# Kernel tuning notes

Hardware: AMD Instinct MI355X
Metric: run time of the kernel (lower is better)

The kernel has to match this reference:

```python
import jax, jax.numpy as jnp
import numpy as np
from math import factorial

LMAX = 4
N_COEFF = (LMAX + 1) ** 2      # 25 real spherical-harmonic coefficients
N_RADII = 300                  # distance_bins
N_NODES = 512
FEAT = 128
RES_BETA, RES_ALPHA = 180, 360
DIST_STEP = 0.05


def _sh_basis(lmax, y, alpha):
    """Real spherical harmonics evaluated on a (beta, alpha) product grid.
    y = cos(beta) quadrature nodes. Returns [res_beta, res_alpha, (lmax+1)^2]."""
    B, A = len(y), len(alpha)
    P = np.zeros((lmax + 1, lmax + 1, B))
    P[0, 0] = 1.0
    s = np.sqrt(np.clip(1.0 - y * y, 0.0, None))
    for m in range(1, lmax + 1):
        P[m, m] = -(2 * m - 1) * s * P[m - 1, m - 1]
    for m in range(lmax):
        P[m + 1, m] = (2 * m + 1) * y * P[m, m]
    for m in range(lmax + 1):
        for l in range(m + 2, lmax + 1):
            P[l, m] = ((2 * l - 1) * y * P[l - 1, m] - (l + m - 1) * P[l - 2, m]) / (l - m)
    cols = []
    for l in range(lmax + 1):
        for m in range(-l, l + 1):
            am = abs(m)
            Nlm = np.sqrt((2 * l + 1) / (4 * np.pi) * factorial(l - am) / factorial(l + am))
            if m == 0:
                col = Nlm * P[l, 0][:, None] * np.ones((1, A))
            elif m > 0:
                col = np.sqrt(2.0) * Nlm * P[l, m][:, None] * np.cos(m * alpha)[None, :]
            else:
                col = np.sqrt(2.0) * Nlm * P[l, am][:, None] * np.sin(am * alpha)[None, :]
            cols.append(col)
    return np.stack(cols, axis=-1).astype(np.float32)


def setup_inputs() -> dict:
    key = jax.random.key(0)
    ks = jax.random.split(key, 14)

    def lin(k, a, b):
        return jax.random.normal(k, (a, b), jnp.float32) / np.float32(np.sqrt(a))

    x = jax.random.normal(ks[0], (N_NODES, FEAT), jnp.float32)
    fd = [FEAT, 128, 128, 64, 16, 2]
    td = [FEAT, 128, 128, 128, 128, 128, 6]
    fW = [lin(ks[1 + i], fd[i], fd[i + 1]) for i in range(5)]
    tW = [lin(ks[6 + i], td[i], td[i + 1]) for i in range(6)]
    pos_w = lin(ks[12], 2 * FEAT, N_RADII * N_COEFF)
    type_emb = jax.random.normal(ks[13], (5, FEAT), jnp.float32)

    y_np, w_np = np.polynomial.legendre.leggauss(RES_BETA)
    alpha_np = np.linspace(0.0, 2.0 * np.pi, RES_ALPHA, endpoint=False)
    basis = jnp.asarray(_sh_basis(LMAX, y_np, alpha_np))          # [B, A, C]
    qw = jnp.asarray(w_np / 2.0, jnp.float32)                     # gausslegendre / 2
    y_grid = jnp.asarray(y_np, jnp.float32)
    alpha_grid = jnp.asarray(alpha_np, jnp.float32)

    return {
        "x": x,
        "focus_w1": fW[0], "focus_w2": fW[1], "focus_w3": fW[2], "focus_w4": fW[3], "focus_w5": fW[4],
        "type_w1": tW[0], "type_w2": tW[1], "type_w3": tW[2], "type_w4": tW[3], "type_w5": tW[4], "type_w6": tW[5],
        "pos_w": pos_w, "type_emb": type_emb,
        "basis": basis, "qw": qw, "y_grid": y_grid, "alpha_grid": alpha_grid,
        "res_beta": RES_BETA, "res_alpha": RES_ALPHA,
    }


def reference(x, focus_w1, focus_w2, focus_w3, focus_w4, focus_w5,
              type_w1, type_w2, type_w3, type_w4, type_w5, type_w6,
              pos_w, type_emb, basis, qw, y_grid, alpha_grid,
              res_beta, res_alpha):
    n_nodes = x.shape[0]

    # --- focus MLP (relu), per-node logits; STOP logit 0 appended ---
    h = x
    for W in (focus_w1, focus_w2, focus_w3, focus_w4):
        h = jax.nn.relu(h @ W)
    focus_scores = (h @ focus_w5)[:, 0]                             # [n_nodes]
    focus_probs = jax.nn.softmax(jnp.concatenate([focus_scores, jnp.zeros((1,), x.dtype)]))
    focus = jnp.minimum(jnp.argmax(focus_probs), n_nodes - 1)

    # --- type MLP (softplus) on the focus node's features ---
    feat_f = x[focus]                                               # [128]
    th = feat_f
    for W in (type_w1, type_w2, type_w3, type_w4, type_w5):
        th = jax.nn.softplus(th @ W)
    type_dist = jax.nn.softmax(th @ type_w6)                        # [6]
    type_idx = jnp.minimum(jnp.argmax(type_dist), 4)

    # --- position head: SH coefficients per radial shell ---
    pos_in = jnp.concatenate([feat_f, type_emb[type_idx]])          # [256]
    coeffs = (pos_in @ pos_w).reshape(N_RADII, N_COEFF)             # [R, C]

    # to_s2grid: log-density on the sphere for every radial shell
    f = jnp.einsum('rc,bac->rba', coeffs, basis)                    # [R, B, A]
    log_meas = jnp.log(qw)[:, None] + jnp.log(2.0 * jnp.pi / res_alpha)  # [B, 1]

    # radial distribution: integral of exp(f) over the sphere, per shell
    log_radial = jax.nn.logsumexp(f + log_meas[None], axis=(1, 2))  # [R]
    radial_probs = jax.nn.softmax(log_radial)

    key = jax.random.key(42)
    k_r, k_a = jax.random.split(key)
    r_idx = jax.random.categorical(k_r, log_radial)

    # angular distribution at the sampled radius, normalized on S2
    fr = f[r_idx]                                                   # [B, A]
    logZr = jax.nn.logsumexp(fr + log_meas)
    angular_dist = jnp.exp(fr - logZr)                              # [B, A]

    joint_log = (fr + log_meas - logZr).reshape(-1)
    idx = jax.random.categorical(k_a, joint_log)
    y_i = idx // res_alpha
    a_i = idx % res_alpha

    radius_pred = (r_idx.astype(jnp.float32) + 1.0) * DIST_STEP
    return (type_dist, radial_probs, angular_dist, radius_pred, y_grid[y_i], alpha_grid[a_i])
```

## Files before the change

kernel.cpp:

```cpp
#include <hip/hip_runtime.h>
#include <math.h>
#include <stdint.h>

#define NNODES 512
#define FEAT   128
#define NR     300
#define NC     25
#define NB     180
#define NA     360
#define RSPLIT 4
#define BCHUNK (NB / RSPLIT)
#define O_TYPE   0
#define O_RAD    6
#define O_ANG    306
#define O_RADIUS 65106
#define O_Y      65107
#define O_ALPHA  65108

#define WS_KEYS   0
#define WS_FOCUS  4
#define WS_TYPEI  5
#define WS_RIDX   6
#define WS_INVZ   7
#define WS_DEAD   8
#define WS_SCORES 320
#define WS_POSIN  832
#define WS_PSUM   1088
#define WS_PV     1280
#define WS_PI     1472
#define WS_Q      1664
#define WS_HR     6176
#define WS_COEF   8352
#define WS_LRP    15872

#define GB_MLP   NNODES
#define GB_PREP  36
#define GB_PFT   162
#define GB_PFP   768
#define GB_TOTAL (GB_MLP + GB_PREP + GB_PFT + GB_PFP)

__constant__ int c_m_of_c[25] = {0,-1,0,1,-2,-1,0,1,2,-3,-2,-1,0,1,2,3,-4,-3,-2,-1,0,1,2,3,4};
__constant__ int c_h_cnt[9] = {5,4,3,2,1,4,3,2,1};
__constant__ int c_h_idx[9][5] = {
  {0,2,6,12,20},
  {3,7,13,21,0},
  {8,14,22,0,0},
  {15,23,0,0,0},
  {24,0,0,0,0},
  {1,5,11,19,0},
  {4,10,18,0,0},
  {9,17,0,0,0},
  {16,0,0,0,0}};

__device__ __forceinline__ void tf2x32(uint32_t k0, uint32_t k1, uint32_t x0, uint32_t x1,
                                       uint32_t& o0, uint32_t& o1) {
  uint32_t ks2 = k0 ^ k1 ^ 0x1BD11BDAu;
#define TF_RND(r) { x0 += x1; x1 = (x1 << r) | (x1 >> (32 - r)); x1 ^= x0; }
  x0 += k0; x1 += k1;
  TF_RND(13) TF_RND(15) TF_RND(26) TF_RND(6)
  x0 += k1; x1 += ks2 + 1u;
  TF_RND(17) TF_RND(29) TF_RND(16) TF_RND(24)
  x0 += ks2; x1 += k0 + 2u;
  TF_RND(13) TF_RND(15) TF_RND(26) TF_RND(6)
  x0 += k0; x1 += k1 + 3u;
  TF_RND(17) TF_RND(29) TF_RND(16) TF_RND(24)
  x0 += k1; x1 += ks2 + 4u;
  TF_RND(13) TF_RND(15) TF_RND(26) TF_RND(6)
  x0 += ks2; x1 += k0 + 5u;
#undef TF_RND
  o0 = x0; o1 = x1;
}

__device__ __forceinline__ float gumbel32(uint32_t k0, uint32_t k1, uint32_t lo) {
  uint32_t o0, o1; tf2x32(k0, k1, 0u, lo, o0, o1);
  uint32_t bits = o0 ^ o1;
  float u = __uint_as_float((bits >> 9) | 0x3f800000u) - 1.0f;
  u = fmaxf(u, 1.1754944e-38f);
  return -logf(-logf(u));
}

__global__ __launch_bounds__(128) void k_front(const float* __restrict__ x,
    const float* __restrict__ w1, const float* __restrict__ w2, const float* __restrict__ w3,
    const float* __restrict__ w4, const float* __restrict__ w5,
    const float* __restrict__ basis, const float* __restrict__ alpha_grid,
    const float* __restrict__ tw1, const float* __restrict__ tw2, const float* __restrict__ tw3,
    const float* __restrict__ tw4, const float* __restrict__ tw5, const float* __restrict__ tw6,
    const float* __restrict__ pos_w,
    float* __restrict__ wsf) {
  int bx = blockIdx.x;
  if (bx >= GB_MLP + GB_PREP + GB_PFT) {
    int pb = bx - (GB_MLP + GB_PREP + GB_PFT);
    const float4* p4 = (const float4*)pos_w;
    const int n4 = NR * NC * 256 / 4;
    float acc = 0.f;
    for (int i = pb * 128 + threadIdx.x; i < n4; i += GB_PFP * 128) {
      float4 v = p4[i];
      acc += v.x + v.y + v.z + v.w;
    }
    if (acc == -1.2345678e30f) wsf[WS_DEAD] = acc;
    return;
  }
  if (bx >= GB_MLP + GB_PREP) {
    int pb = bx - (GB_MLP + GB_PREP);
    int base = pb * 128;
    float acc = 0.f;
    int i = base + threadIdx.x;
    const float4* mats[5] = {(const float4*)tw1, (const float4*)tw2, (const float4*)tw3,
                             (const float4*)tw4, (const float4*)tw5};
    int mi = pb >> 5;
    if (mi < 5) {
      int li = (pb & 31) * 128 + threadIdx.x;
      float4 v = mats[mi][li];
      acc += v.x + v.y + v.z + v.w;
    } else {
      int li = (pb - 160) * 128 + threadIdx.x;
      if (li < 192) { float4 v = ((const float4*)tw6)[li]; acc += v.x + v.y + v.z + v.w; }
    }
    (void)i;
    if (acc == -1.2345678e30f) wsf[WS_DEAD] = acc;
    return;
  }
  if (bx >= GB_MLP) {
    int t = (bx - GB_MLP) * 128 + threadIdx.x;
    if (bx == GB_MLP && threadIdx.x == 0) {
      uint32_t* wu = (uint32_t*)wsf;
      uint32_t o0, o1;
      tf2x32(0u, 42u, 0u, 0u, o0, o1); wu[WS_KEYS + 0] = o0; wu[WS_KEYS + 1] = o1;
      tf2x32(0u, 42u, 0u, 1u, o0, o1); wu[WS_KEYS + 2] = o0; wu[WS_KEYS + 3] = o1;
    }
    if (t < NB * NC) {
      int b = t / NC, c = t % NC;
      int m = c_m_of_c[c];
      float q;
      if (m >= 0) {
        q = basis[(b * NA + 0) * NC + c];
      } else {
        float a10 = alpha_grid[10];
        q = basis[(b * NA + 10) * NC + c] / sinf((float)(-m) * a10);
      }
      wsf[WS_Q + t] = q;
    }
    return;
  }
  __shared__ float ha[128], hb[128];
  int n = bx, j = threadIdx.x;
  ha[j] = x[n * FEAT + j];
  __syncthreads();
  float acc = 0.f;
#pragma unroll 8
  for (int k = 0; k < 128; k++) acc += ha[k] * w1[k * 128 + j];
  hb[j] = fmaxf(acc, 0.f);
  __syncthreads();
  acc = 0.f;
#pragma unroll 8
  for (int k = 0; k < 128; k++) acc += hb[k] * w2[k * 128 + j];
  ha[j] = fmaxf(acc, 0.f);
  __syncthreads();
  if (j < 64) {
    acc = 0.f;
#pragma unroll 8
    for (int k = 0; k < 128; k++) acc += ha[k] * w3[k * 64 + j];
    hb[j] = fmaxf(acc, 0.f);
  }
  __syncthreads();
  if (j < 16) {
    acc = 0.f;
#pragma unroll
    for (int k = 0; k < 64; k++) acc += hb[k] * w4[k * 16 + j];
    ha[j] = fmaxf(acc, 0.f);
  }
  __syncthreads();
  if (j == 0) {
    acc = 0.f;
#pragma unroll
    for (int k = 0; k < 16; k++) acc += ha[k] * w5[k * 2 + 0];
    wsf[WS_SCORES + n] = acc;
  }
}

__global__ __launch_bounds__(1024) void k_type(const float* __restrict__ x,
    const float* __restrict__ w1, const float* __restrict__ w2, const float* __restrict__ w3,
    const float* __restrict__ w4, const float* __restrict__ w5, const float* __restrict__ w6,
    const float* __restrict__ type_emb, float* __restrict__ out, float* __restrict__ wsf) {
  __shared__ float src[128];
  __shared__ float partial[8][128];
  __shared__ float wrv[16]; __shared__ int wri[16];
  __shared__ float lg[6];
  __shared__ int f_sh, ti_sh;
  int t = threadIdx.x;
  int lane = t & 63, wid = t >> 6;
  float bv = -INFINITY; int bi = 1 << 30;
  if (t < NNODES + 1) { bv = (t < NNODES) ? wsf[WS_SCORES + t] : 0.f; bi = t; }
  for (int off = 32; off; off >>= 1) {
    float v2 = __shfl_down(bv, off); int i2 = __shfl_down(bi, off);
    if (v2 > bv || (v2 == bv && i2 < bi)) { bv = v2; bi = i2; }
  }
  if (lane == 0) { wrv[wid] = bv; wri[wid] = bi; }
  __syncthreads();
  if (t == 0) {
    float v0 = wrv[0]; int i0 = wri[0];
    for (int w = 1; w < 16; w++)
      if (wrv[w] > v0 || (wrv[w] == v0 && wri[w] < i0)) { v0 = wrv[w]; i0 = wri[w]; }
    int focus = (i0 < NNODES - 1) ? i0 : (NNODES - 1);
    ((int*)wsf)[WS_FOCUS] = focus;
    f_sh = focus;
  }
  __syncthreads();
  int focus = f_sh;
  if (t < 128) { float xv = x[focus * FEAT + t]; src[t] = xv; wsf[WS_POSIN + t] = xv; }
  __syncthreads();
  const float* Ws[5] = {w1, w2, w3, w4, w5};
#pragma unroll
  for (int L = 0; L < 5; L++) {
    const float* W = Ws[L];
    int j = t & 127, kc = t >> 7;
    float acc = 0.f;
#pragma unroll
    for (int k = 0; k < 16; k++) acc += src[kc * 16 + k] * W[(kc * 16 + k) * 128 + j];
    partial[kc][j] = acc;
    __syncthreads();
    if (t < 128) {
      float s = 0.f;
#pragma unroll
      for (int q = 0; q < 8; q++) s += partial[q][t];
      src[t] = fmaxf(s, 0.f) + log1pf(expf(-fabsf(s)));
    }
    __syncthreads();
  }
  float prod = 0.f;
  if (t < 768) { int o = t >> 7, j = t & 127; prod = src[j] * w6[j * 6 + o]; }
  for (int off = 32; off; off >>= 1) prod += __shfl_down(prod, off);
  if (t < 768 && lane == 0) wrv[wid] = prod;
  __syncthreads();
  if (t == 0) {
    for (int o = 0; o < 6; o++) lg[o] = wrv[2 * o] + wrv[2 * o + 1];
    float M = lg[0]; int am = 0;
    for (int i = 1; i < 6; i++) if (lg[i] > M) { M = lg[i]; am = i; }
    float e[6], S = 0.f;
    for (int i = 0; i < 6; i++) { e[i] = expf(lg[i] - M); S += e[i]; }
    for (int i = 0; i < 6; i++) out[O_TYPE + i] = e[i] / S;
    int ti = (am < 4) ? am : 4;
    ((int*)wsf)[WS_TYPEI] = ti;
    ti_sh = ti;
  }
  __syncthreads();
  if (t < 128) wsf[WS_POSIN + 128 + t] = type_emb[ti_sh * FEAT + t];
}

__global__ __launch_bounds__(256) void k_coeffs(const float* __restrict__ pos_w,
                                                float* __restrict__ wsf) {
  __shared__ float pin[256];
  __shared__ float partial[4][64];
  int t = threadIdx.x;
  pin[t] = wsf[WS_POSIN + t];
  __syncthreads();
  int oL = t & 63, kc = t >> 6;
  int o = blockIdx.x * 64 + oL;
  float acc = 0.f;
  if (o < NR * NC) {
#pragma unroll 16
    for (int k = 0; k < 64; k++) acc += pin[kc * 64 + k] * pos_w[(kc * 64 + k) * (NR * NC) + o];
  }
  partial[kc][oL] = acc;
  __syncthreads();
  if (kc == 0 && o < NR * NC)
    wsf[WS_COEF + o] = partial[0][oL] + partial[1][oL] + partial[2][oL] + partial[3][oL];
}

__global__ __launch_bounds__(384) void k_radial_lse(const float* __restrict__ qw,
    const float* __restrict__ alpha_grid, float* __restrict__ wsf) {
  __shared__ float4 Hs4[BCHUNK * 3];
  __shared__ float cs[NC];
  __shared__ float wred[6];
  int bx = blockIdx.x;
  int r = bx >> 2, s = bx & 3;
  int b0 = s * BCHUNK;
  int t = threadIdx.x;
  float* Hs = (float*)Hs4;
  if (t < NC) cs[t] = wsf[WS_COEF + r * NC + t];
  __syncthreads();
  const float LOGM = -4.0482054576f;
  for (int p = t; p < BCHUNK * 9; p += 384) {
    int b = p / 9, jj = p % 9;
    int bg = b0 + b;
    int n = c_h_cnt[jj];
    float acc = 0.f;
    for (int q = 0; q < n; q++) { int c = c_h_idx[jj][q]; acc += cs[c] * wsf[WS_Q + bg * NC + c]; }
    if (jj == 0) acc += logf(qw[bg]) + LOGM;
    Hs[b * 12 + jj] = acc;
  }
  __syncthreads();
  int a = t;
  float c1 = 0, c2 = 0, c3 = 0, c4 = 0, s1 = 0, s2 = 0, s3 = 0, s4 = 0;
  bool act = a < NA;
  if (act) {
    float al = alpha_grid[a];
    sincosf(al, &s1, &c1);
    sincosf(2.f * al, &s2, &c2);
    sincosf(3.f * al, &s3, &c3);
    sincosf(4.f * al, &s4, &c4);
  }
  float acc = 0.f;
#pragma unroll 5
  for (int b = 0; b < BCHUNK; b++) {
    float4 h0 = Hs4[b * 3 + 0], h1 = Hs4[b * 3 + 1], h2 = Hs4[b * 3 + 2];
    float f = h0.x + h0.y * c1 + h0.z * c2 + h0.w * c3 + h1.x * c4
            + h1.y * s1 + h1.z * s2 + h1.w * s3 + h2.x * s4;
    acc += act ? __expf(f) : 0.f;
  }
  for (int off = 32; off; off >>= 1) acc += __shfl_down(acc, off);
  int wid = t >> 6, lane = t & 63;
  if (lane == 0) wred[wid] = acc;
  __syncthreads();
  if (t == 0) {
    float ss = 0.f;
    for (int w = 0; w < 6; w++) ss += wred[w];
    wsf[WS_LRP + bx] = ss;
  }
}

__global__ __launch_bounds__(256) void k_radial_sample(float* __restrict__ out,
                                                       float* __restrict__ wsf) {
  __shared__ float ssh[NR], lrsh[NR];
  __shared__ float wr[4]; __shared__ int wi[4];
  __shared__ float Ssh; __shared__ int rsh;
  int t = threadIdx.x;
  const uint32_t* wu = (const uint32_t*)wsf;
  uint32_t kr0 = wu[WS_KEYS + 0], kr1 = wu[WS_KEYS + 1];
  for (int i = t; i < NR; i += 256) {
    float s = wsf[WS_LRP + i * 4] + wsf[WS_LRP + i * 4 + 1]
            + wsf[WS_LRP + i * 4 + 2] + wsf[WS_LRP + i * 4 + 3];
    ssh[i] = s;
    lrsh[i] = logf(s);
  }
  __syncthreads();
  float ss = 0.f;
  for (int i = t; i < NR; i += 256) ss += ssh[i];
  for (int off = 32; off; off >>= 1) ss += __shfl_down(ss, off);
  if ((t & 63) == 0) wr[t >> 6] = ss;
  __syncthreads();
  if (t == 0) Ssh = wr[0] + wr[1] + wr[2] + wr[3];
  __syncthreads();
  float S = Ssh;
  for (int i = t; i < NR; i += 256) out[O_RAD + i] = ssh[i] / S;
  float bv = -INFINITY; int bi = 1 << 30;
  for (int i = t; i < NR; i += 256) {
    float v = lrsh[i] + gumbel32(kr0, kr1, (uint32_t)i);
    if (v > bv || (v == bv && i < bi)) { bv = v; bi = i; }
  }
  for (int off = 32; off; off >>= 1) {
    float v2 = __shfl_down(bv, off); int i2 = __shfl_down(bi, off);
    if (v2 > bv || (v2 == bv && i2 < bi)) { bv = v2; bi = i2; }
  }
  if ((t & 63) == 0) { wr[t >> 6] = bv; wi[t >> 6] = bi; }
  __syncthreads();
  if (t == 0) {
    float v0 = wr[0]; int i0 = wi[0];
    for (int w = 1; w < 4; w++)
      if (wr[w] > v0 || (wr[w] == v0 && wi[w] < i0)) { v0 = wr[w]; i0 = wi[w]; }
    rsh = i0;
    ((int*)wsf)[WS_RIDX] = i0;
    out[O_RADIUS] = (float)(i0 + 1) * 0.05f;
  }
  __syncthreads();
  int r = rsh;
  for (int p = t; p < NB * 9; p += 256) {
    int b = p / 9, jj = p % 9, n = c_h_cnt[jj];
    float acc = 0.f;
    for (int q = 0; q < n; q++) {
      int c = c_h_idx[jj][q];
      acc += wsf[WS_COEF + r * NC + c] * wsf[WS_Q + b * NC + c];
    }
    wsf[WS_HR + b * 12 + jj] = acc;
  }
}

__global__ __launch_bounds__(384) void k_ang_partial(const float* __restrict__ qw,
    const float* __restrict__ alpha_grid, float* __restrict__ out, float* __restrict__ wsf) {
  __shared__ float wred[6]; __shared__ float wrv[6]; __shared__ int wri[6];
  int b = blockIdx.x, t = threadIdx.x;
  const uint32_t* wu = (const uint32_t*)wsf;
  uint32_t ka0 = wu[WS_KEYS + 2], ka1 = wu[WS_KEYS + 3];
  const float4* hr4 = (const float4*)(wsf + WS_HR + b * 12);
  float4 h0 = hr4[0], h1 = hr4[1], h2 = hr4[2];
  const float MEAS = 0.01745329252f;
  float elm = qw[b] * MEAS;
  float lm = logf(elm);
  float e = 0.f, v = -INFINITY; int idx = b * NA + t;
  if (t < NA) {
    float al = alpha_grid[t];
    float s1, c1, s2, c2, s3, c3, s4, c4;
    sincosf(al, &s1, &c1); sincosf(2.f * al, &s2, &c2);
    sincosf(3.f * al, &s3, &c3); sincosf(4.f * al, &s4, &c4);
    float f = h0.x + h0.y * c1 + h0.z * c2 + h0.w * c3 + h1.x * c4
            + h1.y * s1 + h1.z * s2 + h1.w * s3 + h2.x * s4;
    float ef = __expf(f);
    out[O_ANG + idx] = ef;
    e = ef * elm;
    v = f + lm + gumbel32(ka0, ka1, (uint32_t)idx);
  }
  int wid = t >> 6, lane = t & 63;
  for (int off = 32; off; off >>= 1) e += __shfl_down(e, off);
  if (lane == 0) wred[wid] = e;
  for (int off = 32; off; off >>= 1) {
    float v2 = __shfl_down(v, off); int i2 = __shfl_down(idx, off);
    if (v2 > v || (v2 == v && i2 < idx)) { v = v2; idx = i2; }
  }
  if (lane == 0) { wrv[wid] = v; wri[wid] = idx; }
  __syncthreads();
  if (t == 0) {
    float zs = 0.f;
    float v0 = wrv[0]; int i0 = wri[0];
    for (int w = 0; w < 6; w++) {
      zs += wred[w];
      if (w && (wrv[w] > v0 || (wrv[w] == v0 && wri[w] < i0))) { v0 = wrv[w]; i0 = wri[w]; }
    }
    wsf[WS_PSUM + b] = zs;
    wsf[WS_PV + b] = v0;
    ((int*)wsf)[WS_PI + b] = i0;
  }
}

__global__ __launch_bounds__(256) void k_ang_final(const float* __restrict__ y_grid,
    const float* __restrict__ alpha_grid, float* __restrict__ out, float* __restrict__ wsf) {
  __shared__ float wr[4]; __shared__ int wi[4];
  int t = threadIdx.x;
  float sv = (t < NB) ? wsf[WS_PSUM + t] : 0.f;
  for (int off = 32; off; off >>= 1) sv += __shfl_down(sv, off);
  if ((t & 63) == 0) wr[t >> 6] = sv;
  __syncthreads();
  if (t == 0) wsf[WS_INVZ] = 1.0f / (wr[0] + wr[1] + wr[2] + wr[3]);
  __syncthreads();
  float v = (t < NB) ? wsf[WS_PV + t] : -INFINITY;
  int i = (t < NB) ? ((const int*)wsf)[WS_PI + t] : (1 << 30);
  for (int off = 32; off; off >>= 1) {
    float v2 = __shfl_down(v, off); int i2 = __shfl_down(i, off);
    if (v2 > v || (v2 == v && i2 < i)) { v = v2; i = i2; }
  }
  if ((t & 63) == 0) { wr[t >> 6] = v; wi[t >> 6] = i; }
  __syncthreads();
  if (t == 0) {
    float v0 = wr[0]; int i0 = wi[0];
    for (int w = 1; w < 4; w++)
      if (wr[w] > v0 || (wr[w] == v0 && wi[w] < i0)) { v0 = wr[w]; i0 = wi[w]; }
    int yi = i0 / NA, ai = i0 % NA;
    out[O_Y] = y_grid[yi];
    out[O_ALPHA] = alpha_grid[ai];
  }
}

__global__ __launch_bounds__(256) void k_ang_scale(float* __restrict__ out,
                                                   const float* __restrict__ wsf) {
  int i = blockIdx.x * 256 + threadIdx.x;
  float invZ = wsf[WS_INVZ];
  if (i < NB * NA) out[O_ANG + i] *= invZ;
}

extern "C" void kernel_launch(void* const* d_in, const int* in_sizes, int n_in,
                              void* d_out, int out_size, void* d_ws, size_t ws_size,
                              hipStream_t stream) {
  const float* x          = (const float*)d_in[0];
  const float* fw1        = (const float*)d_in[1];
  const float* fw2        = (const float*)d_in[2];
  const float* fw3        = (const float*)d_in[3];
  const float* fw4        = (const float*)d_in[4];
  const float* fw5        = (const float*)d_in[5];
  const float* tw1        = (const float*)d_in[6];
  const float* tw2        = (const float*)d_in[7];
  const float* tw3        = (const float*)d_in[8];
  const float* tw4        = (const float*)d_in[9];
  const float* tw5        = (const float*)d_in[10];
  const float* tw6        = (const float*)d_in[11];
  const float* pos_w      = (const float*)d_in[12];
  const float* type_emb   = (const float*)d_in[13];
  const float* basis      = (const float*)d_in[14];
  const float* qw         = (const float*)d_in[15];
  const float* y_grid     = (const float*)d_in[16];
  const float* alpha_grid = (const float*)d_in[17];
  (void)in_sizes; (void)n_in; (void)out_size; (void)ws_size;
  float* out = (float*)d_out;
  float* wsf = (float*)d_ws;

  k_front<<<GB_TOTAL, 128, 0, stream>>>(x, fw1, fw2, fw3, fw4, fw5, basis, alpha_grid,
                                        tw1, tw2, tw3, tw4, tw5, tw6, pos_w, wsf);
  k_type<<<1, 1024, 0, stream>>>(x, tw1, tw2, tw3, tw4, tw5, tw6, type_emb, out, wsf);
  k_coeffs<<<(NR * NC + 63) / 64, 256, 0, stream>>>(pos_w, wsf);
  k_radial_lse<<<NR * RSPLIT, 384, 0, stream>>>(qw, alpha_grid, wsf);
  k_radial_sample<<<1, 256, 0, stream>>>(out, wsf);
  k_ang_partial<<<NB, 384, 0, stream>>>(qw, alpha_grid, out, wsf);
  k_ang_final<<<1, 256, 0, stream>>>(y_grid, alpha_grid, out, wsf);
  k_ang_scale<<<(NB * NA + 255) / 256, 256, 0, stream>>>(out, wsf);
}
```

Before: 65.84 us.

## Fuse eight launches into three using last-block atomic counters and spin-wait flag

```diff
diff --git a/kernel.cpp b/kernel.cpp
--- a/kernel.cpp
+++ b/kernel.cpp
@@ -8,7 +8,7 @@
 #define NC     25
 #define NB     180
 #define NA     360
-#define RSPLIT 4
+#define RSPLIT 2
 #define BCHUNK (NB / RSPLIT)
 #define O_TYPE   0
 #define O_RAD    6
@@ -21,23 +21,22 @@
 #define WS_FOCUS  4
 #define WS_TYPEI  5
 #define WS_RIDX   6
-#define WS_INVZ   7
 #define WS_DEAD   8
-#define WS_SCORES 320
-#define WS_POSIN  832
-#define WS_PSUM   1088
-#define WS_PV     1280
-#define WS_PI     1472
-#define WS_Q      1664
-#define WS_HR     6176
-#define WS_COEF   8352
-#define WS_LRP    15872
-
-#define GB_MLP   NNODES
-#define GB_PREP  36
-#define GB_PFT   162
-#define GB_PFP   768
-#define GB_TOTAL (GB_MLP + GB_PREP + GB_PFT + GB_PFP)
+#define WS_CNT    48
+#define WS_SCORES 64
+#define WS_POSIN  576
+#define WS_PSUM   832
+#define WS_PV     1012
+#define WS_PI     1192
+#define WS_Q      1376
+#define WS_HR     5888
+#define WS_LRP    8064
+
+#define G1_MLP   64
+#define G1_PREP  18
+#define G1_PFT   21
+#define G1_PFP   240
+#define G1_TOTAL (G1_MLP + G1_PREP + G1_PFT + G1_PFP)
 
 __constant__ int c_m_of_c[25] = {0,-1,0,1,-2,-1,0,1,2,-3,-2,-1,0,1,2,3,-4,-3,-2,-1,0,1,2,3,4};
 __constant__ int c_h_cnt[9] = {5,4,3,2,1,4,3,2,1};
@@ -79,57 +78,101 @@
   return -logf(-logf(u));
 }
 
-__global__ __launch_bounds__(128) void k_front(const float* __restrict__ x,
+__device__ __forceinline__ bool last_block(float* wsf, int cidx, int total, int* lds_go) {
+  __threadfence();
+  __syncthreads();
+  if (threadIdx.x == 0) {
+    unsigned int old = atomicAdd((unsigned int*)wsf + WS_CNT + cidx, 1u);
+    *lds_go = (old == (unsigned int)(total - 1)) ? 1 : 0;
+  }
+  __syncthreads();
+  return *lds_go != 0;
+}
+
+__global__ __launch_bounds__(256) void k_front(const float* __restrict__ x,
     const float* __restrict__ w1, const float* __restrict__ w2, const float* __restrict__ w3,
     const float* __restrict__ w4, const float* __restrict__ w5,
     const float* __restrict__ basis, const float* __restrict__ alpha_grid,
     const float* __restrict__ tw1, const float* __restrict__ tw2, const float* __restrict__ tw3,
     const float* __restrict__ tw4, const float* __restrict__ tw5, const float* __restrict__ tw6,
-    const float* __restrict__ pos_w,
-    float* __restrict__ wsf) {
-  int bx = blockIdx.x;
-  if (bx >= GB_MLP + GB_PREP + GB_PFT) {
-    int pb = bx - (GB_MLP + GB_PREP + GB_PFT);
-    const float4* p4 = (const float4*)pos_w;
-    const int n4 = NR * NC * 256 / 4;
-    float acc = 0.f;
-    for (int i = pb * 128 + threadIdx.x; i < n4; i += GB_PFP * 128) {
-      float4 v = p4[i];
-      acc += v.x + v.y + v.z + v.w;
-    }
-    if (acc == -1.2345678e30f) wsf[WS_DEAD] = acc;
-    return;
-  }
-  if (bx >= GB_MLP + GB_PREP) {
-    int pb = bx - (GB_MLP + GB_PREP);
-    int base = pb * 128;
-    float acc = 0.f;
-    int i = base + threadIdx.x;
-    const float4* mats[5] = {(const float4*)tw1, (const float4*)tw2, (const float4*)tw3,
-                             (const float4*)tw4, (const float4*)tw5};
-    int mi = pb >> 5;
-    if (mi < 5) {
-      int li = (pb & 31) * 128 + threadIdx.x;
-      float4 v = mats[mi][li];
-      acc += v.x + v.y + v.z + v.w;
-    } else {
-      int li = (pb - 160) * 128 + threadIdx.x;
-      if (li < 192) { float4 v = ((const float4*)tw6)[li]; acc += v.x + v.y + v.z + v.w; }
-    }
-    (void)i;
-    if (acc == -1.2345678e30f) wsf[WS_DEAD] = acc;
-    return;
-  }
-  if (bx >= GB_MLP) {
-    int t = (bx - GB_MLP) * 128 + threadIdx.x;
-    if (bx == GB_MLP && threadIdx.x == 0) {
+    const float* __restrict__ pos_w, const float* __restrict__ type_emb,
+    float* __restrict__ out, float* __restrict__ wsf) {
+  __shared__ float A[8][128];
+  __shared__ float B[8][128];
+  __shared__ float wv4[4]; __shared__ int wi4[4];
+  __shared__ float lg2[2][6];
+  __shared__ int go_sh, f_sh, ti_sh;
+  int bx = blockIdx.x, t = threadIdx.x;
+
+  if (bx < G1_MLP) {
+    int base = bx * 8;
+    for (int i = t; i < 8 * 128; i += 256) A[i >> 7][i & 127] = x[(base + (i >> 7)) * FEAT + (i & 127)];
+    __syncthreads();
+    int j = t & 127, h = t >> 7;
+    {
+      float a0 = 0, a1 = 0, a2 = 0, a3 = 0;
+#pragma unroll 8
+      for (int k = 0; k < 128; k++) {
+        float wv = w1[k * 128 + j];
+        a0 += A[h * 4 + 0][k] * wv; a1 += A[h * 4 + 1][k] * wv;
+        a2 += A[h * 4 + 2][k] * wv; a3 += A[h * 4 + 3][k] * wv;
+      }
+      __syncthreads();
+      B[h * 4 + 0][j] = fmaxf(a0, 0.f); B[h * 4 + 1][j] = fmaxf(a1, 0.f);
+      B[h * 4 + 2][j] = fmaxf(a2, 0.f); B[h * 4 + 3][j] = fmaxf(a3, 0.f);
+      __syncthreads();
+    }
+    {
+      float a0 = 0, a1 = 0, a2 = 0, a3 = 0;
+#pragma unroll 8
+      for (int k = 0; k < 128; k++) {
+        float wv = w2[k * 128 + j];
+        a0 += B[h * 4 + 0][k] * wv; a1 += B[h * 4 + 1][k] * wv;
+        a2 += B[h * 4 + 2][k] * wv; a3 += B[h * 4 + 3][k] * wv;
+      }
+      __syncthreads();
+      A[h * 4 + 0][j] = fmaxf(a0, 0.f); A[h * 4 + 1][j] = fmaxf(a1, 0.f);
+      A[h * 4 + 2][j] = fmaxf(a2, 0.f); A[h * 4 + 3][j] = fmaxf(a3, 0.f);
+      __syncthreads();
+    }
+    {
+      int j3 = t & 63, g = t >> 6;
+      float a0 = 0, a1 = 0;
+#pragma unroll 8
+      for (int k = 0; k < 128; k++) {
+        float wv = w3[k * 64 + j3];
+        a0 += A[g * 2 + 0][k] * wv; a1 += A[g * 2 + 1][k] * wv;
+      }
+      __syncthreads();
+      B[g * 2 + 0][j3] = fmaxf(a0, 0.f); B[g * 2 + 1][j3] = fmaxf(a1, 0.f);
+      __syncthreads();
+    }
+    {
+      int j4 = t & 15, g4 = t >> 4;
+      if (g4 < 8) {
+        float a0 = 0;
+#pragma unroll
+        for (int k = 0; k < 64; k++) a0 += B[g4][k] * w4[k * 16 + j4];
+        A[g4][j4] = fmaxf(a0, 0.f);
+      }
+      __syncthreads();
+    }
+    if (t < 8) {
+      float a0 = 0;
+#pragma unroll
+      for (int k = 0; k < 16; k++) a0 += A[t][k] * w5[k * 2 + 0];
+      wsf[WS_SCORES + base + t] = a0;
+    }
+  } else if (bx < G1_MLP + G1_PREP) {
+    int p = (bx - G1_MLP) * 256 + t;
+    if (bx == G1_MLP && t == 0) {
       uint32_t* wu = (uint32_t*)wsf;
       uint32_t o0, o1;
       tf2x32(0u, 42u, 0u, 0u, o0, o1); wu[WS_KEYS + 0] = o0; wu[WS_KEYS + 1] = o1;
       tf2x32(0u, 42u, 0u, 1u, o0, o1); wu[WS_KEYS + 2] = o0; wu[WS_KEYS + 3] = o1;
     }
-    if (t < NB * NC) {
-      int b = t / NC, c = t % NC;
+    if (p < NB * NC) {
+      int b = p / NC, c = p % NC;
       int m = c_m_of_c[c];
       float q;
       if (m >= 0) {
@@ -138,102 +181,91 @@
         float a10 = alpha_grid[10];
         q = basis[(b * NA + 10) * NC + c] / sinf((float)(-m) * a10);
       }
-      wsf[WS_Q + t] = q;
-    }
-    return;
-  }
-  __shared__ float ha[128], hb[128];
-  int n = bx, j = threadIdx.x;
-  ha[j] = x[n * FEAT + j];
-  __syncthreads();
-  float acc = 0.f;
-#pragma unroll 8
-  for (int k = 0; k < 128; k++) acc += ha[k] * w1[k * 128 + j];
-  hb[j] = fmaxf(acc, 0.f);
-  __syncthreads();
-  acc = 0.f;
-#pragma unroll 8
-  for (int k = 0; k < 128; k++) acc += hb[k] * w2[k * 128 + j];
-  ha[j] = fmaxf(acc, 0.f);
-  __syncthreads();
-  if (j < 64) {
-    acc = 0.f;
-#pragma unroll 8
-    for (int k = 0; k < 128; k++) acc += ha[k] * w3[k * 64 + j];
-    hb[j] = fmaxf(acc, 0.f);
-  }
-  __syncthreads();
-  if (j < 16) {
-    acc = 0.f;
-#pragma unroll
-    for (int k = 0; k < 64; k++) acc += hb[k] * w4[k * 16 + j];
-    ha[j] = fmaxf(acc, 0.f);
-  }
-  __syncthreads();
-  if (j == 0) {
-    acc = 0.f;
-#pragma unroll
-    for (int k = 0; k < 16; k++) acc += ha[k] * w5[k * 2 + 0];
-    wsf[WS_SCORES + n] = acc;
-  }
-}
-
-__global__ __launch_bounds__(1024) void k_type(const float* __restrict__ x,
-    const float* __restrict__ w1, const float* __restrict__ w2, const float* __restrict__ w3,
-    const float* __restrict__ w4, const float* __restrict__ w5, const float* __restrict__ w6,
-    const float* __restrict__ type_emb, float* __restrict__ out, float* __restrict__ wsf) {
-  __shared__ float src[128];
-  __shared__ float partial[8][128];
-  __shared__ float wrv[16]; __shared__ int wri[16];
-  __shared__ float lg[6];
-  __shared__ int f_sh, ti_sh;
-  int t = threadIdx.x;
+      wsf[WS_Q + p] = q;
+    }
+  } else if (bx < G1_MLP + G1_PREP + G1_PFT) {
+    const float4* mats[5] = {(const float4*)tw1, (const float4*)tw2, (const float4*)tw3,
+                             (const float4*)tw4, (const float4*)tw5};
+    int lid = (bx - (G1_MLP + G1_PREP)) * 256 + t;
+    float acc = 0.f;
+    for (int vi = lid; vi < 20672; vi += G1_PFT * 256) {
+      int mi = vi >> 12;
+      float4 v;
+      if (mi < 5) v = mats[mi][vi & 4095];
+      else        v = ((const float4*)tw6)[vi - 20480];
+      acc += v.x + v.y + v.z + v.w;
+    }
+    if (acc == -1.2345678e30f) wsf[WS_DEAD] = acc;
+  } else {
+    int lid = (bx - (G1_MLP + G1_PREP + G1_PFT)) * 256 + t;
+    const float4* p4 = (const float4*)pos_w;
+    float acc = 0.f;
+    for (int i = lid; i < NR * NC * 256 / 4; i += G1_PFP * 256) {
+      float4 v = p4[i];
+      acc += v.x + v.y + v.z + v.w;
+    }
+    if (acc == -1.2345678e30f) wsf[WS_DEAD] = acc;
+  }
+
+  if (!last_block(wsf, 0, G1_TOTAL, &go_sh)) return;
+  __threadfence();
   int lane = t & 63, wid = t >> 6;
   float bv = -INFINITY; int bi = 1 << 30;
-  if (t < NNODES + 1) { bv = (t < NNODES) ? wsf[WS_SCORES + t] : 0.f; bi = t; }
+  for (int i = t; i < NNODES + 1; i += 256) {
+    float v = (i < NNODES) ? wsf[WS_SCORES + i] : 0.f;
+    if (v > bv || (v == bv && i < bi)) { bv = v; bi = i; }
+  }
   for (int off = 32; off; off >>= 1) {
     float v2 = __shfl_down(bv, off); int i2 = __shfl_down(bi, off);
     if (v2 > bv || (v2 == bv && i2 < bi)) { bv = v2; bi = i2; }
   }
-  if (lane == 0) { wrv[wid] = bv; wri[wid] = bi; }
+  if (lane == 0) { wv4[wid] = bv; wi4[wid] = bi; }
   __syncthreads();
   if (t == 0) {
-    float v0 = wrv[0]; int i0 = wri[0];
-    for (int w = 1; w < 16; w++)
-      if (wrv[w] > v0 || (wrv[w] == v0 && wri[w] < i0)) { v0 = wrv[w]; i0 = wri[w]; }
+    float v0 = wv4[0]; int i0 = wi4[0];
+    for (int w = 1; w < 4; w++)
+      if (wv4[w] > v0 || (wv4[w] == v0 && wi4[w] < i0)) { v0 = wv4[w]; i0 = wi4[w]; }
     int focus = (i0 < NNODES - 1) ? i0 : (NNODES - 1);
     ((int*)wsf)[WS_FOCUS] = focus;
     f_sh = focus;
   }
   __syncthreads();
   int focus = f_sh;
+  float* src = &A[0][0];
   if (t < 128) { float xv = x[focus * FEAT + t]; src[t] = xv; wsf[WS_POSIN + t] = xv; }
   __syncthreads();
-  const float* Ws[5] = {w1, w2, w3, w4, w5};
+  const float* Ws[5] = {tw1, tw2, tw3, tw4, tw5};
+  int kc = t >> 7, j = t & 127;
 #pragma unroll
   for (int L = 0; L < 5; L++) {
     const float* W = Ws[L];
-    int j = t & 127, kc = t >> 7;
-    float acc = 0.f;
-#pragma unroll
-    for (int k = 0; k < 16; k++) acc += src[kc * 16 + k] * W[(kc * 16 + k) * 128 + j];
-    partial[kc][j] = acc;
+    float acc = 0.f;
+#pragma unroll 8
+    for (int k = 0; k < 64; k++) { int kk = kc * 64 + k; acc += src[kk] * W[kk * 128 + j]; }
+    B[kc][j] = acc;
     __syncthreads();
     if (t < 128) {
-      float s = 0.f;
-#pragma unroll
-      for (int q = 0; q < 8; q++) s += partial[q][t];
+      float s = B[0][t] + B[1][t];
       src[t] = fmaxf(s, 0.f) + log1pf(expf(-fabsf(s)));
     }
     __syncthreads();
   }
-  float prod = 0.f;
-  if (t < 768) { int o = t >> 7, j = t & 127; prod = src[j] * w6[j * 6 + o]; }
-  for (int off = 32; off; off >>= 1) prod += __shfl_down(prod, off);
-  if (t < 768 && lane == 0) wrv[wid] = prod;
+  float pr[6] = {0, 0, 0, 0, 0, 0};
+  if (t < 128) {
+    float sv = src[t];
+#pragma unroll
+    for (int o = 0; o < 6; o++) pr[o] = sv * tw6[t * 6 + o];
+  }
+#pragma unroll
+  for (int o = 0; o < 6; o++)
+    for (int off = 32; off; off >>= 1) pr[o] += __shfl_down(pr[o], off);
+  if (t < 128 && lane == 0)
+#pragma unroll
+    for (int o = 0; o < 6; o++) lg2[wid][o] = pr[o];
   __syncthreads();
   if (t == 0) {
-    for (int o = 0; o < 6; o++) lg[o] = wrv[2 * o] + wrv[2 * o + 1];
+    float lg[6];
+    for (int o = 0; o < 6; o++) lg[o] = lg2[0][o] + lg2[1][o];
     float M = lg[0]; int am = 0;
     for (int i = 1; i < 6; i++) if (lg[i] > M) { M = lg[i]; am = i; }
     float e[6], S = 0.f;
@@ -247,37 +279,38 @@
   if (t < 128) wsf[WS_POSIN + 128 + t] = type_emb[ti_sh * FEAT + t];
 }
 
-__global__ __launch_bounds__(256) void k_coeffs(const float* __restrict__ pos_w,
-                                                float* __restrict__ wsf) {
+__global__ __launch_bounds__(384) void k_sphere(const float* __restrict__ pos_w,
+    const float* __restrict__ qw, const float* __restrict__ alpha_grid,
+    float* __restrict__ out, float* __restrict__ wsf) {
   __shared__ float pin[256];
-  __shared__ float partial[4][64];
-  int t = threadIdx.x;
-  pin[t] = wsf[WS_POSIN + t];
-  __syncthreads();
-  int oL = t & 63, kc = t >> 6;
-  int o = blockIdx.x * 64 + oL;
-  float acc = 0.f;
-  if (o < NR * NC) {
-#pragma unroll 16
-    for (int k = 0; k < 64; k++) acc += pin[kc * 64 + k] * pos_w[(kc * 64 + k) * (NR * NC) + o];
-  }
-  partial[kc][oL] = acc;
-  __syncthreads();
-  if (kc == 0 && o < NR * NC)
-    wsf[WS_COEF + o] = partial[0][oL] + partial[1][oL] + partial[2][oL] + partial[3][oL];
-}
-
-__global__ __launch_bounds__(384) void k_radial_lse(const float* __restrict__ qw,
-    const float* __restrict__ alpha_grid, float* __restrict__ wsf) {
+  __shared__ float part[12][32];
+  __shared__ float cs[NC];
   __shared__ float4 Hs4[BCHUNK * 3];
-  __shared__ float cs[NC];
-  __shared__ float wred[6];
-  int bx = blockIdx.x;
-  int r = bx >> 2, s = bx & 3;
-  int b0 = s * BCHUNK;
-  int t = threadIdx.x;
+  __shared__ float wred[6]; __shared__ int wri[6];
+  __shared__ float fss[NR], flr[NR];
+  __shared__ float S_sh; __shared__ int go_sh, r_sh;
+  int bx = blockIdx.x, t = threadIdx.x;
+  int r = bx >> 1, s = bx & 1, b0 = s * BCHUNK;
   float* Hs = (float*)Hs4;
-  if (t < NC) cs[t] = wsf[WS_COEF + r * NC + t];
+  if (t < 256) pin[t] = wsf[WS_POSIN + t];
+  __syncthreads();
+  {
+    int kk = t >> 5, c = t & 31;
+    float acc = 0.f;
+    if (c < NC) {
+      const float* col = pos_w + r * NC + c;
+#pragma unroll 4
+      for (int k = kk; k < 256; k += 12) acc += pin[k] * col[k * (NR * NC)];
+    }
+    part[kk][c] = acc;
+  }
+  __syncthreads();
+  if (t < NC) {
+    float a = 0.f;
+#pragma unroll
+    for (int kk = 0; kk < 12; kk++) a += part[kk][t];
+    cs[t] = a;
+  }
   __syncthreads();
   const float LOGM = -4.0482054576f;
   for (int p = t; p < BCHUNK * 9; p += 384) {
@@ -290,95 +323,114 @@
     Hs[b * 12 + jj] = acc;
   }
   __syncthreads();
-  int a = t;
-  float c1 = 0, c2 = 0, c3 = 0, c4 = 0, s1 = 0, s2 = 0, s3 = 0, s4 = 0;
-  bool act = a < NA;
-  if (act) {
-    float al = alpha_grid[a];
-    sincosf(al, &s1, &c1);
-    sincosf(2.f * al, &s2, &c2);
-    sincosf(3.f * al, &s3, &c3);
-    sincosf(4.f * al, &s4, &c4);
-  }
-  float acc = 0.f;
+  int lane = t & 63, wid = t >> 6;
+  {
+    float c1 = 0, c2 = 0, c3 = 0, c4 = 0, s1 = 0, s2 = 0, s3 = 0, s4 = 0;
+    bool act = t < NA;
+    if (act) {
+      float al = alpha_grid[t];
+      sincosf(al, &s1, &c1);
+      sincosf(2.f * al, &s2, &c2);
+      sincosf(3.f * al, &s3, &c3);
+      sincosf(4.f * al, &s4, &c4);
+    }
+    float acc = 0.f;
 #pragma unroll 5
-  for (int b = 0; b < BCHUNK; b++) {
-    float4 h0 = Hs4[b * 3 + 0], h1 = Hs4[b * 3 + 1], h2 = Hs4[b * 3 + 2];
-    float f = h0.x + h0.y * c1 + h0.z * c2 + h0.w * c3 + h1.x * c4
-            + h1.y * s1 + h1.z * s2 + h1.w * s3 + h2.x * s4;
-    acc += act ? __expf(f) : 0.f;
-  }
-  for (int off = 32; off; off >>= 1) acc += __shfl_down(acc, off);
-  int wid = t >> 6, lane = t & 63;
-  if (lane == 0) wred[wid] = acc;
-  __syncthreads();
-  if (t == 0) {
-    float ss = 0.f;
-    for (int w = 0; w < 6; w++) ss += wred[w];
-    wsf[WS_LRP + bx] = ss;
-  }
-}
-
-__global__ __launch_bounds__(256) void k_radial_sample(float* __restrict__ out,
-                                                       float* __restrict__ wsf) {
-  __shared__ float ssh[NR], lrsh[NR];
-  __shared__ float wr[4]; __shared__ int wi[4];
-  __shared__ float Ssh; __shared__ int rsh;
-  int t = threadIdx.x;
+    for (int b = 0; b < BCHUNK; b++) {
+      float4 h0 = Hs4[b * 3 + 0], h1 = Hs4[b * 3 + 1], h2 = Hs4[b * 3 + 2];
+      float f = h0.x + h0.y * c1 + h0.z * c2 + h0.w * c3 + h1.x * c4
+              + h1.y * s1 + h1.z * s2 + h1.w * s3 + h2.x * s4;
+      acc += act ? __expf(f) : 0.f;
+    }
+    for (int off = 32; off; off >>= 1) acc += __shfl_down(acc, off);
+    if (lane == 0) wred[wid] = acc;
+    __syncthreads();
+    if (t == 0) {
+      float ss = 0.f;
+      for (int w = 0; w < 6; w++) ss += wred[w];
+      wsf[WS_LRP + bx] = ss;
+    }
+  }
+  if (!last_block(wsf, 1, NR * RSPLIT, &go_sh)) return;
+  __threadfence();
   const uint32_t* wu = (const uint32_t*)wsf;
   uint32_t kr0 = wu[WS_KEYS + 0], kr1 = wu[WS_KEYS + 1];
-  for (int i = t; i < NR; i += 256) {
-    float s = wsf[WS_LRP + i * 4] + wsf[WS_LRP + i * 4 + 1]
-            + wsf[WS_LRP + i * 4 + 2] + wsf[WS_LRP + i * 4 + 3];
-    ssh[i] = s;
-    lrsh[i] = logf(s);
-  }
-  __syncthreads();
-  float ss = 0.f;
-  for (int i = t; i < NR; i += 256) ss += ssh[i];
-  for (int off = 32; off; off >>= 1) ss += __shfl_down(ss, off);
-  if ((t & 63) == 0) wr[t >> 6] = ss;
-  __syncthreads();
-  if (t == 0) Ssh = wr[0] + wr[1] + wr[2] + wr[3];
-  __syncthreads();
-  float S = Ssh;
-  for (int i = t; i < NR; i += 256) out[O_RAD + i] = ssh[i] / S;
-  float bv = -INFINITY; int bi = 1 << 30;
-  for (int i = t; i < NR; i += 256) {
-    float v = lrsh[i] + gumbel32(kr0, kr1, (uint32_t)i);
-    if (v > bv || (v == bv && i < bi)) { bv = v; bi = i; }
-  }
-  for (int off = 32; off; off >>= 1) {
-    float v2 = __shfl_down(bv, off); int i2 = __shfl_down(bi, off);
-    if (v2 > bv || (v2 == bv && i2 < bi)) { bv = v2; bi = i2; }
-  }
-  if ((t & 63) == 0) { wr[t >> 6] = bv; wi[t >> 6] = bi; }
-  __syncthreads();
-  if (t == 0) {
-    float v0 = wr[0]; int i0 = wi[0];
-    for (int w = 1; w < 4; w++)
-      if (wr[w] > v0 || (wr[w] == v0 && wi[w] < i0)) { v0 = wr[w]; i0 = wi[w]; }
-    rsh = i0;
-    ((int*)wsf)[WS_RIDX] = i0;
-    out[O_RADIUS] = (float)(i0 + 1) * 0.05f;
-  }
-  __syncthreads();
-  int r = rsh;
-  for (int p = t; p < NB * 9; p += 256) {
+  float sv = 0.f, lr = -INFINITY;
+  if (t < NR) {
+    sv = wsf[WS_LRP + 2 * t] + wsf[WS_LRP + 2 * t + 1];
+    lr = logf(sv);
+    fss[t] = sv; flr[t] = lr;
+  }
+  {
+    float ss = sv;
+    for (int off = 32; off; off >>= 1) ss += __shfl_down(ss, off);
+    if (lane == 0) wred[wid] = ss;
+    __syncthreads();
+    if (t == 0) {
+      float S = 0.f;
+      for (int w = 0; w < 6; w++) S += wred[w];
+      S_sh = S;
+    }
+    __syncthreads();
+  }
+  if (t < NR) out[O_RAD + t] = sv / S_sh;
+  {
+    float v = (t < NR) ? lr + gumbel32(kr0, kr1, (uint32_t)t) : -INFINITY;
+    int bi = (t < NR) ? t : (1 << 30);
+    for (int off = 32; off; off >>= 1) {
+      float v2 = __shfl_down(v, off); int i2 = __shfl_down(bi, off);
+      if (v2 > v || (v2 == v && i2 < bi)) { v = v2; bi = i2; }
+    }
+    if (lane == 0) { wred[wid] = v; wri[wid] = bi; }
+    __syncthreads();
+    if (t == 0) {
+      float v0 = wred[0]; int i0 = wri[0];
+      for (int w = 1; w < 6; w++)
+        if (wred[w] > v0 || (wred[w] == v0 && wri[w] < i0)) { v0 = wred[w]; i0 = wri[w]; }
+      r_sh = i0;
+      ((int*)wsf)[WS_RIDX] = i0;
+      out[O_RADIUS] = (float)(i0 + 1) * 0.05f;
+    }
+    __syncthreads();
+  }
+  int rr = r_sh;
+  __syncthreads();
+  {
+    int kk = t >> 5, c = t & 31;
+    float acc = 0.f;
+    if (c < NC) {
+      const float* col = pos_w + rr * NC + c;
+#pragma unroll 4
+      for (int k = kk; k < 256; k += 12) acc += pin[k] * col[k * (NR * NC)];
+    }
+    part[kk][c] = acc;
+  }
+  __syncthreads();
+  if (t < NC) {
+    float a = 0.f;
+#pragma unroll
+    for (int kk = 0; kk < 12; kk++) a += part[kk][t];
+    cs[t] = a;
+  }
+  __syncthreads();
+  for (int p = t; p < NB * 9; p += 384) {
     int b = p / 9, jj = p % 9, n = c_h_cnt[jj];
     float acc = 0.f;
     for (int q = 0; q < n; q++) {
       int c = c_h_idx[jj][q];
-      acc += wsf[WS_COEF + r * NC + c] * wsf[WS_Q + b * NC + c];
+      acc += cs[c] * wsf[WS_Q + b * NC + c];
     }
     wsf[WS_HR + b * 12 + jj] = acc;
   }
 }
 
-__global__ __launch_bounds__(384) void k_ang_partial(const float* __restrict__ qw,
-    const float* __restrict__ alpha_grid, float* __restrict__ out, float* __restrict__ wsf) {
+__global__ __launch_bounds__(384) void k_ang(const float* __restrict__ qw,
+    const float* __restrict__ alpha_grid, const float* __restrict__ y_grid,
+    float* __restrict__ out, float* __restrict__ wsf) {
   __shared__ float wred[6]; __shared__ float wrv[6]; __shared__ int wri[6];
+  __shared__ int go_sh; __shared__ float invz_sh;
   int b = blockIdx.x, t = threadIdx.x;
+  int lane = t & 63, wid = t >> 6;
   const uint32_t* wu = (const uint32_t*)wsf;
   uint32_t ka0 = wu[WS_KEYS + 2], ka1 = wu[WS_KEYS + 3];
   const float4* hr4 = (const float4*)(wsf + WS_HR + b * 12);
@@ -386,7 +438,7 @@
   const float MEAS = 0.01745329252f;
   float elm = qw[b] * MEAS;
   float lm = logf(elm);
-  float e = 0.f, v = -INFINITY; int idx = b * NA + t;
+  float ef = 0.f, e = 0.f, v = -INFINITY; int idx = (t < NA) ? b * NA + t : (1 << 30);
   if (t < NA) {
     float al = alpha_grid[t];
     float s1, c1, s2, c2, s3, c3, s4, c4;
@@ -394,12 +446,10 @@
     sincosf(3.f * al, &s3, &c3); sincosf(4.f * al, &s4, &c4);
     float f = h0.x + h0.y * c1 + h0.z * c2 + h0.w * c3 + h1.x * c4
             + h1.y * s1 + h1.z * s2 + h1.w * s3 + h2.x * s4;
-    float ef = __expf(f);
-    out[O_ANG + idx] = ef;
+    ef = __expf(f);
     e = ef * elm;
     v = f + lm + gumbel32(ka0, ka1, (uint32_t)idx);
   }
-  int wid = t >> 6, lane = t & 63;
   for (int off = 32; off; off >>= 1) e += __shfl_down(e, off);
   if (lane == 0) wred[wid] = e;
   for (int off = 32; off; off >>= 1) {
@@ -419,41 +469,43 @@
     wsf[WS_PV + b] = v0;
     ((int*)wsf)[WS_PI + b] = i0;
   }
-}
-
-__global__ __launch_bounds__(256) void k_ang_final(const float* __restrict__ y_grid,
-    const float* __restrict__ alpha_grid, float* __restrict__ out, float* __restrict__ wsf) {
-  __shared__ float wr[4]; __shared__ int wi[4];
-  int t = threadIdx.x;
-  float sv = (t < NB) ? wsf[WS_PSUM + t] : 0.f;
-  for (int off = 32; off; off >>= 1) sv += __shfl_down(sv, off);
-  if ((t & 63) == 0) wr[t >> 6] = sv;
-  __syncthreads();
-  if (t == 0) wsf[WS_INVZ] = 1.0f / (wr[0] + wr[1] + wr[2] + wr[3]);
-  __syncthreads();
-  float v = (t < NB) ? wsf[WS_PV + t] : -INFINITY;
-  int i = (t < NB) ? ((const int*)wsf)[WS_PI + t] : (1 << 30);
-  for (int off = 32; off; off >>= 1) {
-    float v2 = __shfl_down(v, off); int i2 = __shfl_down(i, off);
-    if (v2 > v || (v2 == v && i2 < i)) { v = v2; i = i2; }
-  }
-  if ((t & 63) == 0) { wr[t >> 6] = v; wi[t >> 6] = i; }
-  __syncthreads();
+  unsigned int* flagp = (unsigned int*)wsf + WS_CNT + 3;
+  if (last_block(wsf, 2, NB, &go_sh)) {
+    __threadfence();
+    float sv = (t < NB) ? wsf[WS_PSUM + t] : 0.f;
+    for (int off = 32; off; off >>= 1) sv += __shfl_down(sv, off);
+    if (lane == 0) wred[wid] = sv;
+    float vv = (t < NB) ? wsf[WS_PV + t] : -INFINITY;
+    int ii = (t < NB) ? ((const int*)wsf)[WS_PI + t] : (1 << 30);
+    for (int off = 32; off; off >>= 1) {
+      float v2 = __shfl_down(vv, off); int i2 = __shfl_down(ii, off);
+      if (v2 > vv || (v2 == vv && i2 < ii)) { vv = v2; ii = i2; }
+    }
+    if (lane == 0) { wrv[wid] = vv; wri[wid] = ii; }
+    __syncthreads();
+    if (t == 0) {
+      float Z = 0.f;
+      float v0 = wrv[0]; int i0 = wri[0];
+      for (int w = 0; w < 6; w++) {
+        Z += wred[w];
+        if (w && (wrv[w] > v0 || (wrv[w] == v0 && wri[w] < i0))) { v0 = wrv[w]; i0 = wri[w]; }
+      }
+      int yi = i0 / NA, ai = i0 % NA;
+      out[O_Y] = y_grid[yi];
+      out[O_ALPHA] = alpha_grid[ai];
+      float invZ = 1.0f / Z;
+      __threadfence();
+      __hip_atomic_store(flagp, __float_as_uint(invZ), __ATOMIC_RELEASE, __HIP_MEMORY_SCOPE_AGENT);
+    }
+  }
   if (t == 0) {
-    float v0 = wr[0]; int i0 = wi[0];
-    for (int w = 1; w < 4; w++)
-      if (wr[w] > v0 || (wr[w] == v0 && wi[w] < i0)) { v0 = wr[w]; i0 = wi[w]; }
-    int yi = i0 / NA, ai = i0 % NA;
-    out[O_Y] = y_grid[yi];
-    out[O_ALPHA] = alpha_grid[ai];
-  }
-}
-
-__global__ __launch_bounds__(256) void k_ang_scale(float* __restrict__ out,
-                                                   const float* __restrict__ wsf) {
-  int i = blockIdx.x * 256 + threadIdx.x;
-  float invZ = wsf[WS_INVZ];
-  if (i < NB * NA) out[O_ANG + i] *= invZ;
+    unsigned int u;
+    while ((u = __hip_atomic_load(flagp, __ATOMIC_ACQUIRE, __HIP_MEMORY_SCOPE_AGENT)) == 0u)
+      __builtin_amdgcn_s_sleep(8);
+    invz_sh = __uint_as_float(u);
+  }
+  __syncthreads();
+  if (t < NA) out[O_ANG + b * NA + t] = ef * invz_sh;
 }
 
 extern "C" void kernel_launch(void* const* d_in, const int* in_sizes, int n_in,
@@ -481,13 +533,10 @@
   float* out = (float*)d_out;
   float* wsf = (float*)d_ws;
 
-  k_front<<<GB_TOTAL, 128, 0, stream>>>(x, fw1, fw2, fw3, fw4, fw5, basis, alpha_grid,
-                                        tw1, tw2, tw3, tw4, tw5, tw6, pos_w, wsf);
-  k_type<<<1, 1024, 0, stream>>>(x, tw1, tw2, tw3, tw4, tw5, tw6, type_emb, out, wsf);
-  k_coeffs<<<(NR * NC + 63) / 64, 256, 0, stream>>>(pos_w, wsf);
-  k_radial_lse<<<NR * RSPLIT, 384, 0, stream>>>(qw, alpha_grid, wsf);
-  k_radial_sample<<<1, 256, 0, stream>>>(out, wsf);
-  k_ang_partial<<<NB, 384, 0, stream>>>(qw, alpha_grid, out, wsf);
-  k_ang_final<<<1, 256, 0, stream>>>(y_grid, alpha_grid, out, wsf);
-  k_ang_scale<<<(NB * NA + 255) / 256, 256, 0, stream>>>(out, wsf);
-}
+  hipMemsetAsync((char*)d_ws + WS_CNT * 4, 0, 16, stream);
+  k_front<<<G1_TOTAL, 256, 0, stream>>>(x, fw1, fw2, fw3, fw4, fw5, basis, alpha_grid,
+                                        tw1, tw2, tw3, tw4, tw5, tw6, pos_w, type_emb,
+                                        out, wsf);
+  k_sphere<<<NR * RSPLIT, 384, 0, stream>>>(pos_w, qw, alpha_grid, out, wsf);
+  k_ang<<<NB, 384, 0, stream>>>(qw, alpha_grid, y_grid, out, wsf);
+}
```

Result: slower. 193.4 us (+193.8%).
